# Performance work log

Hardware: AMD Instinct MI355X
Metric: run time of the kernel (lower is better)

## Reference

```python
import jax, jax.numpy as jnp
import numpy as np

N_HEAD = 8


def _axial_attn(x, wq, wk, wv, fw, fb, axis):
    # x: (B, T, H, W, C); axis is the axial axis in (B, nh, T, H, W, d): 2=T, 3=H, 4=W
    B, T, H, W, C = x.shape
    d = C // N_HEAD

    def heads(y):
        # (B,T,H,W,C) -> (B, nh, T, H, W, d)
        return jnp.moveaxis(y.reshape(B, T, H, W, N_HEAD, d), -2, 1)

    q, k, v = heads(x @ wq), heads(x @ wk), heads(x @ wv)
    # restrict attention to the axial axis: move it to -2, all other dims are batch
    q = jnp.moveaxis(q, axis, -2)
    k = jnp.moveaxis(k, axis, -2)
    v = jnp.moveaxis(v, axis, -2)
    scale = 1.0 / jnp.sqrt(jnp.asarray(d, x.dtype))
    scores = jnp.einsum('...ld,...md->...lm', q * scale, k)
    att = jax.nn.softmax(scores, axis=-1)
    o = jnp.einsum('...lm,...md->...ld', att, v)
    o = jnp.moveaxis(o, -2, axis)            # restore axial axis position
    o = jnp.moveaxis(o, 1, -2).reshape(B, T, H, W, C)  # merge heads
    return o @ fw + fb


def setup_inputs() -> dict:
    key = jax.random.key(0)
    ks = jax.random.split(key, 16)
    C = 512
    x = jax.random.normal(ks[0], (4, C, 16, 32, 32), jnp.float32)
    s = 0.02

    def w(k):
        return jax.random.normal(k, (C, C), jnp.float32) * s

    inp = {'x': x}
    i = 1
    for ax in ('w', 'h', 't'):
        inp[f'wq_{ax}'] = w(ks[i])
        inp[f'wk_{ax}'] = w(ks[i + 1])
        inp[f'wv_{ax}'] = w(ks[i + 2])
        inp[f'fc_{ax}'] = w(ks[i + 3])
        inp[f'fb_{ax}'] = jnp.zeros((C,), jnp.float32)
        i += 4
    return inp


def reference(x, wq_w, wk_w, wv_w, fc_w, fb_w,
              wq_h, wk_h, wv_h, fc_h, fb_h,
              wq_t, wk_t, wv_t, fc_t, fb_t):
    xt = jnp.moveaxis(x, 1, -1)  # (B, C, T, H, W) -> (B, T, H, W, C)
    out = (_axial_attn(xt, wq_w, wk_w, wv_w, fc_w, fb_w, 4)   # attend along W
           + _axial_attn(xt, wq_h, wk_h, wv_h, fc_h, fb_h, 3)  # attend along H
           + _axial_attn(xt, wq_t, wk_t, wv_t, fc_t, fb_t, 2))  # attend along T
    return jnp.moveaxis(out, -1, 1)  # back to (B, C, T, H, W)
```

## Files before the change

kernel.cpp:

```cpp
#include <hip/hip_runtime.h>
#include <stdint.h>

typedef __attribute__((ext_vector_type(8))) short bf16x8;
typedef __attribute__((ext_vector_type(4))) float f32x4;

static __device__ __forceinline__ short f2bf(float f) {
  uint32_t u = __builtin_bit_cast(uint32_t, f);
  u += 0x7fffu + ((u >> 16) & 1u);
  return (short)(u >> 16);
}

static __device__ __forceinline__ void gload_lds16(const void* g, void* l) {
  __builtin_amdgcn_global_load_lds((const __attribute__((address_space(1))) void*)g,
                                   (__attribute__((address_space(3))) void*)l, 16, 0, 0);
}

#define GFENCE asm volatile("" ::: "memory")

__global__ __launch_bounds__(256) void transpose_x_k(const float* __restrict__ x,
                                                     short* __restrict__ xb) {
  __shared__ float t[64][65];
  const int pt = blockIdx.x, ct = blockIdx.y, b = blockIdx.z;
  const int tid = threadIdx.x;
#pragma unroll
  for (int i = 0; i < 16; i++) {
    int cc = i * 4 + (tid >> 6);
    int pp = tid & 63;
    t[cc][pp] = x[(size_t)(b * 512 + ct * 64 + cc) * 16384 + pt * 64 + pp];
  }
  __syncthreads();
#pragma unroll
  for (int i = 0; i < 2; i++) {
    int seg = i * 256 + tid;
    int pw = seg >> 3, c8 = seg & 7;
    short tmp[8];
#pragma unroll
    for (int k = 0; k < 8; k++) tmp[k] = f2bf(t[c8 * 8 + k][pw]);
    *(uint4*)&xb[(size_t)(b * 16384 + pt * 64 + pw) * 512 + ct * 64 + c8 * 8] =
        *(const uint4*)tmp;
  }
}

struct WPtrs {
  const float* src[12];
  short* dst[12];
  int ld[12];
};

__global__ __launch_bounds__(256) void transpose_w_k(WPtrs P) {
  __shared__ float t[64][65];
  const int kt = blockIdx.x, nt = blockIdx.y, z = blockIdx.z;
  const float* src = P.src[z];
  short* dst = P.dst[z];
  const int ld = P.ld[z];
  const int tid = threadIdx.x;
#pragma unroll
  for (int i = 0; i < 16; i++) {
    int kk = i * 4 + (tid >> 6);
    int nn = tid & 63;
    t[kk][nn] = src[(kt * 64 + kk) * 512 + nt * 64 + nn];
  }
  __syncthreads();
#pragma unroll
  for (int i = 0; i < 2; i++) {
    int seg = i * 256 + tid;
    int nn = seg >> 3, k8 = seg & 7;
    short tmp[8];
#pragma unroll
    for (int k = 0; k < 8; k++) tmp[k] = f2bf(t[k8 * 8 + k][nn]);
    *(uint4*)&dst[(size_t)(nt * 64 + nn) * ld + kt * 64 + k8 * 8] = *(const uint4*)tmp;
  }
}

__global__ void bsum_k(const float* a, const float* b, const float* c, float* o) {
  int i = blockIdx.x * 256 + threadIdx.x;
  if (i < 512) o[i] = a[i] + b[i] + c[i];
}

#define LOADB(b, kh)                                                           \
  do {                                                                         \
    _Pragma("unroll") for (int ni = 0; ni < 4; ++ni) bfr[ni] =                 \
        *(const bf16x8*)(smem + ((b) * 4 + 2 + (kh)) * 16384 + boff +          \
                         ni * 1024);                                           \
  } while (0)

#define LOADA(b, kh, mq)                                                       \
  do {                                                                         \
    _Pragma("unroll") for (int mi = 0; mi < 4; ++mi) af[mi] =                  \
        *(const bf16x8*)(smem + ((b) * 4 + (kh)) * 16384 + aoff +              \
                         ((mq) * 4 + mi) * 1024);                              \
  } while (0)

#define MFMA16(mq)                                                             \
  do {                                                                         \
    __builtin_amdgcn_s_setprio(1);                                             \
    _Pragma("unroll") for (int mi = 0; mi < 4; ++mi)                           \
        _Pragma("unroll") for (int ni = 0; ni < 4; ++ni) acc[(mq) * 4 + mi]    \
            [ni] = __builtin_amdgcn_mfma_f32_16x16x32_bf16(                    \
                af[mi], bfr[ni], acc[(mq) * 4 + mi][ni], 0, 0, 0);             \
    __builtin_amdgcn_s_setprio(0);                                             \
    GFENCE;                                                                    \
  } while (0)

#define TILE(b, W0, W2, S0, S1, S2, S3)                                        \
  do {                                                                         \
    asm volatile("s_waitcnt vmcnt(" W0 ")" ::: "memory");                      \
    __builtin_amdgcn_s_barrier();                                              \
    GFENCE;                                                                    \
    LOADB(b, 0);                                                               \
    LOADA(b, 0, 0);                                                            \
    S0;                                                                        \
    MFMA16(0);                                                                 \
    __builtin_amdgcn_s_barrier();                                              \
    GFENCE;                                                                    \
    LOADA(b, 0, 1);                                                            \
    S1;                                                                        \
    MFMA16(1);                                                                 \
    asm volatile("s_waitcnt vmcnt(" W2 ")" ::: "memory");                      \
    __builtin_amdgcn_s_barrier();                                              \
    GFENCE;                                                                    \
    LOADB(b, 1);                                                               \
    LOADA(b, 1, 0);                                                            \
    S2;                                                                        \
    MFMA16(0);                                                                 \
    __builtin_amdgcn_s_barrier();                                              \
    GFENCE;                                                                    \
    LOADA(b, 1, 1);                                                            \
    S3;                                                                        \
    MFMA16(1);                                                                 \
  } while (0)

template <int MODE>
__global__ __launch_bounds__(512, 2) void gemm256_k(const short* __restrict__ A,
                                                    int lda,
                                                    const short* __restrict__ B,
                                                    int ldb, void* __restrict__ Dp,
                                                    int K, int ldd,
                                                    const float* __restrict__ bsum,
                                                    int GN) {
  extern __shared__ char smem[];
  const int tid = threadIdx.x;
  const int lane = tid & 63, wave = tid >> 6;
  const int wr = wave >> 2, wc = wave & 3;
  const int r4 = lane & 15, kl = lane >> 4;

  int bid = blockIdx.x;
  const int cpx = gridDim.x >> 3;
  bid = (bid & 7) * cpx + (bid >> 3);
  int bm, bn;
  if constexpr (MODE == 0) {
    bn = bid % GN;
    bm = bid / GN;
  } else {
    bm = bid & 1;
    bn = bid >> 1;
  }

  const int NT = K >> 6;

  const int srow = tid >> 2;
  const int schk = (tid & 3) ^ ((tid >> 4) & 3);
  const short* gA0 = A + (size_t)(bm * 256 + srow) * lda + schk * 8;
  const short* gB0 = B + (size_t)(bn * 256 + srow) * ldb + schk * 8;

  auto stage = [&](int tt, int x) {
    const short* g = (x < 2) ? gA0 : gB0;
    const size_t rstep = (size_t)128 * ((x < 2) ? lda : ldb);
    const size_t koff = (size_t)tt * 64 + (x & 1) * 32;
    char* ldst = smem + (((tt & 1) * 4 + x) * 16384) + wave * 1024;
#pragma unroll
    for (int i = 0; i < 2; ++i)
      gload_lds16(g + i * rstep + koff, ldst + i * 8192);
  };

  const int kls = kl ^ (r4 >> 2);
  const int aoff = wr * 8192 + r4 * 64 + kls * 16;
  const int boff = wc * 4096 + r4 * 64 + kls * 16;

  f32x4 acc[8][4];
#pragma unroll
  for (int i = 0; i < 8; ++i)
#pragma unroll
    for (int j = 0; j < 4; ++j) acc[i][j] = (f32x4){0.f, 0.f, 0.f, 0.f};
  bf16x8 af[4], bfr[4];

  stage(0, 0);
  stage(0, 2);
  stage(0, 1);
  stage(0, 3);
  stage(1, 0);
  stage(1, 2);

  int t = 0;
  for (; t < NT - 2; ++t) {
    const int b = t & 1;
    TILE(b, "8", "8", stage(t + 1, 1), stage(t + 1, 3), stage(t + 2, 0),
         stage(t + 2, 2));
  }
  {
    const int b = t & 1;
    TILE(b, "8", "8", stage(t + 1, 1), stage(t + 1, 3), (void)0, (void)0);
    ++t;
  }
  {
    const int b = t & 1;
    TILE(b, "4", "0", (void)0, (void)0, (void)0, (void)0);
  }

  const int m0 = wr * 128 + kl * 4;
  const int n0 = wc * 64 + r4;
  if (MODE == 0) {
    short* D = (short*)Dp;
#pragma unroll
    for (int mi = 0; mi < 8; ++mi)
#pragma unroll
      for (int ni = 0; ni < 4; ++ni)
#pragma unroll
        for (int r = 0; r < 4; ++r) {
          int row = bm * 256 + m0 + mi * 16 + r;
          int col = bn * 256 + n0 + ni * 16;
          D[(size_t)row * ldd + col] = f2bf(acc[mi][ni][r]);
        }
  } else {
    float* D = (float*)Dp + (size_t)((bn * 256) >> 14) * 8388608;
#pragma unroll
    for (int mi = 0; mi < 8; ++mi)
#pragma unroll
      for (int ni = 0; ni < 4; ++ni)
#pragma unroll
        for (int r = 0; r < 4; ++r) {
          int c = bm * 256 + m0 + mi * 16 + r;
          int n = (bn * 256 + n0 + ni * 16) & 16383;
          if (MODE == 1)
            D[(size_t)c * 16384 + n] = acc[mi][ni][r] + bsum[c];
          else
            D[(size_t)c * 16384 + n] += acc[mi][ni][r];
        }
  }
}

template <int L>
__global__ __launch_bounds__(256) void attn_k(const short* __restrict__ qkv,
                                              short* __restrict__ o, int Adiv, int Bmul,
                                              int Cmul, int stride, int obase,
                                              int ostride) {
  constexpr int R = 256 / L;
  constexpr int SPT = (L * L) / 256;
  constexpr int OPT = 64 / R;
  __shared__ short Ks[L][72];
  __shared__ short Vs[L][72];
  __shared__ short Qs[L][72];
  __shared__ float att[L][L + 1];
  const int tid = threadIdx.x;
  const int blk = blockIdx.x;
  const int s = blk >> 3, head = blk & 7;
  const int base = (s / Adiv) * Bmul + (s % Adiv) * Cmul;

  for (int idx = tid; idx < L * 8 * 3; idx += 256) {
    int part = idx / (L * 8);
    int rem = idx - part * (L * 8);
    int row = rem >> 3, seg = rem & 7;
    int n = base + row * stride;
    uint4 v = *(const uint4*)&qkv[(size_t)n * 1536 + part * 512 + head * 64 + seg * 8];
    short* dst = (part == 0 ? &Qs[row][0] : part == 1 ? &Ks[row][0] : &Vs[row][0]);
    *(uint4*)(dst + seg * 8) = v;
  }
  __syncthreads();

  const int l = tid / R, r = tid % R;
  float q[64];
#pragma unroll
  for (int w = 0; w < 8; w++) {
    uint4 u = *(const uint4*)&Qs[l][w * 8];
    uint32_t arr[4] = {u.x, u.y, u.z, u.w};
#pragma unroll
    for (int p = 0; p < 4; p++) {
      q[w * 8 + p * 2] = __builtin_bit_cast(float, arr[p] << 16);
      q[w * 8 + p * 2 + 1] = __builtin_bit_cast(float, arr[p] & 0xffff0000u);
    }
  }
  float sc[SPT];
#pragma unroll
  for (int jj = 0; jj < SPT; jj++) {
    int j = jj * R + r;
    float a0 = 0.f;
#pragma unroll
    for (int w = 0; w < 8; w++) {
      uint4 u = *(const uint4*)&Ks[j][w * 8];
      uint32_t arr[4] = {u.x, u.y, u.z, u.w};
#pragma unroll
      for (int p = 0; p < 4; p++) {
        a0 += q[w * 8 + p * 2] * __builtin_bit_cast(float, arr[p] << 16);
        a0 += q[w * 8 + p * 2 + 1] * __builtin_bit_cast(float, arr[p] & 0xffff0000u);
      }
    }
    sc[jj] = a0 * 0.125f;
  }
  float mx = sc[0];
#pragma unroll
  for (int jj = 1; jj < SPT; jj++) mx = fmaxf(mx, sc[jj]);
#pragma unroll
  for (int d = 1; d < R; d <<= 1) mx = fmaxf(mx, __shfl_xor(mx, d));
  float p_[SPT];
  float sum = 0.f;
#pragma unroll
  for (int jj = 0; jj < SPT; jj++) {
    p_[jj] = __expf(sc[jj] - mx);
    sum += p_[jj];
  }
#pragma unroll
  for (int d = 1; d < R; d <<= 1) sum += __shfl_xor(sum, d);
  float inv = 1.0f / sum;
#pragma unroll
  for (int jj = 0; jj < SPT; jj++) att[l][jj * R + r] = p_[jj] * inv;
  __syncthreads();

  float oa[OPT] = {};
#pragma unroll 4
  for (int j = 0; j < L; j++) {
    float a = att[l][j];
    if constexpr (OPT == 8) {
      uint4 u = *(const uint4*)&Vs[j][r * 8];
      uint32_t arr[4] = {u.x, u.y, u.z, u.w};
#pragma unroll
      for (int p = 0; p < 4; p++) {
        oa[p * 2] += a * __builtin_bit_cast(float, arr[p] << 16);
        oa[p * 2 + 1] += a * __builtin_bit_cast(float, arr[p] & 0xffff0000u);
      }
    } else {
      uint2 u = *(const uint2*)&Vs[j][r * 4];
      uint32_t arr[2] = {u.x, u.y};
#pragma unroll
      for (int p = 0; p < 2; p++) {
        oa[p * 2] += a * __builtin_bit_cast(float, arr[p] << 16);
        oa[p * 2 + 1] += a * __builtin_bit_cast(float, arr[p] & 0xffff0000u);
      }
    }
  }
  short tmp[OPT];
#pragma unroll
  for (int i = 0; i < OPT; i++) tmp[i] = f2bf(oa[i]);
  int n = base + l * stride;
  if constexpr (OPT == 8)
    *(uint4*)&o[(size_t)n * ostride + obase + head * 64 + r * 8] = *(const uint4*)tmp;
  else
    *(uint2*)&o[(size_t)n * ostride + obase + head * 64 + r * 4] = *(const uint2*)tmp;
}

extern "C" void kernel_launch(void* const* d_in, const int* in_sizes, int n_in,
                              void* d_out, int out_size, void* d_ws, size_t ws_size,
                              hipStream_t stream) {
  const float* x = (const float*)d_in[0];
  const float* wq[3];
  const float* wk[3];
  const float* wv[3];
  const float* fc[3];
  const float* fb[3];
  for (int a = 0; a < 3; a++) {
    wq[a] = (const float*)d_in[1 + a * 5];
    wk[a] = (const float*)d_in[2 + a * 5];
    wv[a] = (const float*)d_in[3 + a * 5];
    fc[a] = (const float*)d_in[4 + a * 5];
    fb[a] = (const float*)d_in[5 + a * 5];
  }
  char* ws = (char*)d_ws;
  short* xb = (short*)(ws);
  short* qkv = (short*)(ws + 67108864);
  short* wqkvt = (short*)(ws + 268435456);
  short* fctA = (short*)(ws + 273154048);
  float* bsum = (float*)(ws + 274726912);
  short* ob = (short*)(ws + 274728960);
  float* out = (float*)d_out;

  const bool fused = ws_size >= 476055552ull;

  (void)hipFuncSetAttribute((const void*)&gemm256_k<0>,
                            hipFuncAttributeMaxDynamicSharedMemorySize, 131072);
  (void)hipFuncSetAttribute((const void*)&gemm256_k<1>,
                            hipFuncAttributeMaxDynamicSharedMemorySize, 131072);
  (void)hipFuncSetAttribute((const void*)&gemm256_k<2>,
                            hipFuncAttributeMaxDynamicSharedMemorySize, 131072);

  WPtrs P;
  for (int a = 0; a < 3; a++) {
    P.src[a * 4 + 0] = wq[a];
    P.src[a * 4 + 1] = wk[a];
    P.src[a * 4 + 2] = wv[a];
    P.src[a * 4 + 3] = fc[a];
    P.dst[a * 4 + 0] = wqkvt + (size_t)a * 1536 * 512;
    P.dst[a * 4 + 1] = wqkvt + (size_t)a * 1536 * 512 + 512 * 512;
    P.dst[a * 4 + 2] = wqkvt + (size_t)a * 1536 * 512 + 2 * 512 * 512;
    P.dst[a * 4 + 3] = fctA + a * 512;
    P.ld[a * 4 + 0] = 512;
    P.ld[a * 4 + 1] = 512;
    P.ld[a * 4 + 2] = 512;
    P.ld[a * 4 + 3] = 1536;
  }
  transpose_w_k<<<dim3(8, 8, 12), 256, 0, stream>>>(P);
  bsum_k<<<dim3(2), 256, 0, stream>>>(fb[0], fb[1], fb[2], bsum);
  transpose_x_k<<<dim3(256, 8, 4), 256, 0, stream>>>(x, xb);

  const int Ad[3] = {1, 32, 1024};
  const int Bm_[3] = {32, 1024, 16384};
  const int Cm[3] = {0, 1, 1};
  const int St[3] = {1, 32, 1024};
  const int Ls[3] = {32, 32, 16};

  for (int a = 0; a < 3; a++) {
    gemm256_k<0><<<dim3(1536), 512, 131072, stream>>>(
        xb, 512, wqkvt + (size_t)a * 1536 * 512, 512, (void*)qkv, 512, 1536,
        nullptr, 6);
    const int obase = fused ? a * 512 : 0;
    const int ostr = fused ? 1536 : 512;
    if (Ls[a] == 32)
      attn_k<32><<<dim3(2048 * 8), 256, 0, stream>>>(qkv, ob, Ad[a], Bm_[a], Cm[a],
                                                     St[a], obase, ostr);
    else
      attn_k<16><<<dim3(4096 * 8), 256, 0, stream>>>(qkv, ob, Ad[a], Bm_[a], Cm[a],
                                                     St[a], obase, ostr);
    if (!fused) {
      if (a == 0)
        gemm256_k<1><<<dim3(512), 512, 131072, stream>>>(
            fctA + a * 512, 1536, ob, 512, (void*)out, 512, 0, bsum, 0);
      else
        gemm256_k<2><<<dim3(512), 512, 131072, stream>>>(
            fctA + a * 512, 1536, ob, 512, (void*)out, 512, 0, bsum, 0);
    }
  }
  if (fused) {
    gemm256_k<1><<<dim3(512), 512, 131072, stream>>>(
        fctA, 1536, ob, 1536, (void*)out, 1536, 0, bsum, 0);
  }
}
```

Baseline: 830.5 us.

## Restructure GEMM mainloop into 4-stage K=32 LDS pipeline with explicit waits

```diff
diff --git a/kernel.cpp b/kernel.cpp
--- a/kernel.cpp
+++ b/kernel.cpp
@@ -77,18 +77,16 @@
   if (i < 512) o[i] = a[i] + b[i] + c[i];
 }
 
-#define LOADB(b, kh)                                                           \
+#define LOADB(q)                                                               \
   do {                                                                         \
     _Pragma("unroll") for (int ni = 0; ni < 4; ++ni) bfr[ni] =                 \
-        *(const bf16x8*)(smem + ((b) * 4 + 2 + (kh)) * 16384 + boff +          \
-                         ni * 1024);                                           \
+        *(const bf16x8*)(smem + (q) * 32768 + 16384 + boff + ni * 1024);       \
   } while (0)
 
-#define LOADA(b, kh, mq)                                                       \
+#define LOADA(q, mq)                                                           \
   do {                                                                         \
     _Pragma("unroll") for (int mi = 0; mi < 4; ++mi) af[mi] =                  \
-        *(const bf16x8*)(smem + ((b) * 4 + (kh)) * 16384 + aoff +              \
-                         ((mq) * 4 + mi) * 1024);                              \
+        *(const bf16x8*)(smem + (q) * 32768 + aoff + ((mq) * 4 + mi) * 1024);  \
   } while (0)
 
 #define MFMA16(mq)                                                             \
@@ -102,33 +100,39 @@
     GFENCE;                                                                    \
   } while (0)
 
-#define TILE(b, W0, W2, S0, S1, S2, S3)                                        \
+#define PH0(q, SA)                                                             \
   do {                                                                         \
-    asm volatile("s_waitcnt vmcnt(" W0 ")" ::: "memory");                      \
+    LOADB(q);                                                                  \
+    LOADA(q, 0);                                                               \
+    SA;                                                                        \
+    GFENCE;                                                                    \
     __builtin_amdgcn_s_barrier();                                              \
-    GFENCE;                                                                    \
-    LOADB(b, 0);                                                               \
-    LOADA(b, 0, 0);                                                            \
-    S0;                                                                        \
+    asm volatile("s_waitcnt lgkmcnt(0)" ::: "memory");                         \
+    __builtin_amdgcn_sched_barrier(0);                                         \
     MFMA16(0);                                                                 \
+    GFENCE;                                                                    \
     __builtin_amdgcn_s_barrier();                                              \
     GFENCE;                                                                    \
-    LOADA(b, 0, 1);                                                            \
-    S1;                                                                        \
+  } while (0)
+
+#define PH1(q, SB, VM)                                                         \
+  do {                                                                         \
+    LOADA(q, 1);                                                               \
+    SB;                                                                        \
+    VM;                                                                        \
+    GFENCE;                                                                    \
+    __builtin_amdgcn_s_barrier();                                              \
+    asm volatile("s_waitcnt lgkmcnt(0)" ::: "memory");                         \
+    __builtin_amdgcn_sched_barrier(0);                                         \
     MFMA16(1);                                                                 \
-    asm volatile("s_waitcnt vmcnt(" W2 ")" ::: "memory");                      \
+    GFENCE;                                                                    \
     __builtin_amdgcn_s_barrier();                                              \
     GFENCE;                                                                    \
-    LOADB(b, 1);                                                               \
-    LOADA(b, 1, 0);                                                            \
-    S2;                                                                        \
-    MFMA16(0);                                                                 \
-    __builtin_amdgcn_s_barrier();                                              \
-    GFENCE;                                                                    \
-    LOADA(b, 1, 1);                                                            \
-    S3;                                                                        \
-    MFMA16(1);                                                                 \
   } while (0)
+
+#define VM8 asm volatile("s_waitcnt vmcnt(8)" ::: "memory")
+#define VM4 asm volatile("s_waitcnt vmcnt(4)" ::: "memory")
+#define VM0 asm volatile("s_waitcnt vmcnt(0)" ::: "memory")
 
 template <int MODE>
 __global__ __launch_bounds__(512, 2) void gemm256_k(const short* __restrict__ A,
@@ -156,7 +160,7 @@
     bn = bid >> 1;
   }
 
-  const int NT = K >> 6;
+  const int NT = K >> 5;
 
   const int srow = tid >> 2;
   const int schk = (tid & 3) ^ ((tid >> 4) & 3);
@@ -164,10 +168,10 @@
   const short* gB0 = B + (size_t)(bn * 256 + srow) * ldb + schk * 8;
 
   auto stage = [&](int tt, int x) {
-    const short* g = (x < 2) ? gA0 : gB0;
-    const size_t rstep = (size_t)128 * ((x < 2) ? lda : ldb);
-    const size_t koff = (size_t)tt * 64 + (x & 1) * 32;
-    char* ldst = smem + (((tt & 1) * 4 + x) * 16384) + wave * 1024;
+    const short* g = x ? gB0 : gA0;
+    const size_t rstep = (size_t)128 * (x ? ldb : lda);
+    const size_t koff = (size_t)tt * 32;
+    char* ldst = smem + (tt & 3) * 32768 + x * 16384 + wave * 1024;
 #pragma unroll
     for (int i = 0; i < 2; ++i)
       gload_lds16(g + i * rstep + koff, ldst + i * 8192);
@@ -185,26 +189,38 @@
   bf16x8 af[4], bfr[4];
 
   stage(0, 0);
-  stage(0, 2);
   stage(0, 1);
-  stage(0, 3);
   stage(1, 0);
-  stage(1, 2);
+  stage(1, 1);
+  stage(2, 0);
+  stage(2, 1);
+  VM8;
+  GFENCE;
+  __builtin_amdgcn_s_barrier();
+  GFENCE;
 
   int t = 0;
-  for (; t < NT - 2; ++t) {
-    const int b = t & 1;
-    TILE(b, "8", "8", stage(t + 1, 1), stage(t + 1, 3), stage(t + 2, 0),
-         stage(t + 2, 2));
+  for (; t < NT - 3; ++t) {
+    const int q = t & 3;
+    PH0(q, stage(t + 3, 0));
+    PH1(q, stage(t + 3, 1), VM8);
   }
   {
-    const int b = t & 1;
-    TILE(b, "8", "8", stage(t + 1, 1), stage(t + 1, 3), (void)0, (void)0);
+    const int q = t & 3;
+    PH0(q, (void)0);
+    PH1(q, (void)0, VM4);
     ++t;
   }
   {
-    const int b = t & 1;
-    TILE(b, "4", "0", (void)0, (void)0, (void)0, (void)0);
+    const int q = t & 3;
+    PH0(q, (void)0);
+    PH1(q, (void)0, VM0);
+    ++t;
+  }
+  {
+    const int q = t & 3;
+    PH0(q, (void)0);
+    PH1(q, (void)0, (void)0);
   }
 
   const int m0 = wr * 128 + kl * 4;
```

Result: no change. 843.0 us (+1.5%).

## Rewrite axial attention with per-wave MFMA tiles and always fuse output projection

Applied to the files above, without the earlier changes.

```diff
diff --git a/kernel.cpp b/kernel.cpp
--- a/kernel.cpp
+++ b/kernel.cpp
@@ -240,111 +240,124 @@
 }
 
 template <int L>
-__global__ __launch_bounds__(256) void attn_k(const short* __restrict__ qkv,
-                                              short* __restrict__ o, int Adiv, int Bmul,
-                                              int Cmul, int stride, int obase,
-                                              int ostride) {
-  constexpr int R = 256 / L;
-  constexpr int SPT = (L * L) / 256;
-  constexpr int OPT = 64 / R;
-  __shared__ short Ks[L][72];
-  __shared__ short Vs[L][72];
-  __shared__ short Qs[L][72];
-  __shared__ float att[L][L + 1];
+__global__ __launch_bounds__(256) void attn_mfma_k(const short* __restrict__ qkv,
+                                                   short* __restrict__ o, int Adiv,
+                                                   int Bmul, int Cmul, int stride,
+                                                   int obase) {
+  constexpr int MT = L / 16;
+  constexpr int PITCH = 40;
+  __shared__ short lds[4 * (32 + 64) * PITCH];
   const int tid = threadIdx.x;
-  const int blk = blockIdx.x;
-  const int s = blk >> 3, head = blk & 7;
+  const int lane = tid & 63, wave = tid >> 6;
+  short* p_lds = lds + wave * (96 * PITCH);
+  short* vt = p_lds + 32 * PITCH;
+
+  const int wid = blockIdx.x * 4 + wave;
+  const int s = wid >> 3, head = wid & 7;
   const int base = (s / Adiv) * Bmul + (s % Adiv) * Cmul;
-
-  for (int idx = tid; idx < L * 8 * 3; idx += 256) {
-    int part = idx / (L * 8);
-    int rem = idx - part * (L * 8);
-    int row = rem >> 3, seg = rem & 7;
-    int n = base + row * stride;
-    uint4 v = *(const uint4*)&qkv[(size_t)n * 1536 + part * 512 + head * 64 + seg * 8];
-    short* dst = (part == 0 ? &Qs[row][0] : part == 1 ? &Ks[row][0] : &Vs[row][0]);
-    *(uint4*)(dst + seg * 8) = v;
-  }
-  __syncthreads();
-
-  const int l = tid / R, r = tid % R;
-  float q[64];
-#pragma unroll
-  for (int w = 0; w < 8; w++) {
-    uint4 u = *(const uint4*)&Qs[l][w * 8];
-    uint32_t arr[4] = {u.x, u.y, u.z, u.w};
-#pragma unroll
-    for (int p = 0; p < 4; p++) {
-      q[w * 8 + p * 2] = __builtin_bit_cast(float, arr[p] << 16);
-      q[w * 8 + p * 2 + 1] = __builtin_bit_cast(float, arr[p] & 0xffff0000u);
+  const int r4 = lane & 15, kl = lane >> 4;
+
+  if constexpr (L == 16) {
+    for (int i = lane; i < 96 * PITCH; i += 64) p_lds[i] = 0;
+  }
+
+  bf16x8 qf[MT][2], kf[MT][2];
+#pragma unroll
+  for (int mi = 0; mi < MT; ++mi)
+#pragma unroll
+    for (int ks = 0; ks < 2; ++ks) {
+      size_t nrow = (size_t)(base + (mi * 16 + r4) * stride) * 1536 + head * 64 +
+                    ks * 32 + kl * 8;
+      qf[mi][ks] = *(const bf16x8*)&qkv[nrow];
+      kf[mi][ks] = *(const bf16x8*)&qkv[nrow + 512];
     }
-  }
-  float sc[SPT];
-#pragma unroll
-  for (int jj = 0; jj < SPT; jj++) {
-    int j = jj * R + r;
-    float a0 = 0.f;
-#pragma unroll
-    for (int w = 0; w < 8; w++) {
-      uint4 u = *(const uint4*)&Ks[j][w * 8];
-      uint32_t arr[4] = {u.x, u.y, u.z, u.w};
-#pragma unroll
-      for (int p = 0; p < 4; p++) {
-        a0 += q[w * 8 + p * 2] * __builtin_bit_cast(float, arr[p] << 16);
-        a0 += q[w * 8 + p * 2 + 1] * __builtin_bit_cast(float, arr[p] & 0xffff0000u);
-      }
+
+#pragma unroll
+  for (int it = 0; it < L / 8; ++it) {
+    int j = (lane >> 3) + it * 8;
+    uint4 u = *(const uint4*)&qkv[(size_t)(base + j * stride) * 1536 + 1024 +
+                                  head * 64 + (lane & 7) * 8];
+    ushort e[8];
+    *(uint4*)e = u;
+#pragma unroll
+    for (int q = 0; q < 8; ++q) vt[((lane & 7) * 8 + q) * PITCH + j] = (short)e[q];
+  }
+
+  f32x4 sacc[MT][MT];
+#pragma unroll
+  for (int i = 0; i < MT; ++i)
+#pragma unroll
+    for (int j = 0; j < MT; ++j) sacc[i][j] = (f32x4){0.f, 0.f, 0.f, 0.f};
+#pragma unroll
+  for (int mi = 0; mi < MT; ++mi)
+#pragma unroll
+    for (int ni = 0; ni < MT; ++ni)
+#pragma unroll
+      for (int ks = 0; ks < 2; ++ks)
+        sacc[mi][ni] = __builtin_amdgcn_mfma_f32_16x16x32_bf16(
+            qf[mi][ks], kf[ni][ks], sacc[mi][ni], 0, 0, 0);
+
+#pragma unroll
+  for (int mi = 0; mi < MT; ++mi) {
+    float mx[4], sm[4];
+#pragma unroll
+    for (int r = 0; r < 4; ++r) {
+      float m = sacc[mi][0][r];
+      if (MT == 2) m = fmaxf(m, sacc[mi][1][r]);
+#pragma unroll
+      for (int d = 1; d < 16; d <<= 1) m = fmaxf(m, __shfl_xor(m, d));
+      mx[r] = m;
     }
-    sc[jj] = a0 * 0.125f;
-  }
-  float mx = sc[0];
-#pragma unroll
-  for (int jj = 1; jj < SPT; jj++) mx = fmaxf(mx, sc[jj]);
-#pragma unroll
-  for (int d = 1; d < R; d <<= 1) mx = fmaxf(mx, __shfl_xor(mx, d));
-  float p_[SPT];
-  float sum = 0.f;
-#pragma unroll
-  for (int jj = 0; jj < SPT; jj++) {
-    p_[jj] = __expf(sc[jj] - mx);
-    sum += p_[jj];
-  }
-#pragma unroll
-  for (int d = 1; d < R; d <<= 1) sum += __shfl_xor(sum, d);
-  float inv = 1.0f / sum;
-#pragma unroll
-  for (int jj = 0; jj < SPT; jj++) att[l][jj * R + r] = p_[jj] * inv;
-  __syncthreads();
-
-  float oa[OPT] = {};
-#pragma unroll 4
-  for (int j = 0; j < L; j++) {
-    float a = att[l][j];
-    if constexpr (OPT == 8) {
-      uint4 u = *(const uint4*)&Vs[j][r * 8];
-      uint32_t arr[4] = {u.x, u.y, u.z, u.w};
-#pragma unroll
-      for (int p = 0; p < 4; p++) {
-        oa[p * 2] += a * __builtin_bit_cast(float, arr[p] << 16);
-        oa[p * 2 + 1] += a * __builtin_bit_cast(float, arr[p] & 0xffff0000u);
-      }
-    } else {
-      uint2 u = *(const uint2*)&Vs[j][r * 4];
-      uint32_t arr[2] = {u.x, u.y};
-#pragma unroll
-      for (int p = 0; p < 2; p++) {
-        oa[p * 2] += a * __builtin_bit_cast(float, arr[p] << 16);
-        oa[p * 2 + 1] += a * __builtin_bit_cast(float, arr[p] & 0xffff0000u);
-      }
+#pragma unroll
+    for (int ni = 0; ni < MT; ++ni)
+#pragma unroll
+      for (int r = 0; r < 4; ++r)
+        sacc[mi][ni][r] = __expf((sacc[mi][ni][r] - mx[r]) * 0.125f);
+#pragma unroll
+    for (int r = 0; r < 4; ++r) {
+      float t = sacc[mi][0][r];
+      if (MT == 2) t += sacc[mi][1][r];
+#pragma unroll
+      for (int d = 1; d < 16; d <<= 1) t += __shfl_xor(t, d);
+      sm[r] = 1.0f / t;
     }
-  }
-  short tmp[OPT];
-#pragma unroll
-  for (int i = 0; i < OPT; i++) tmp[i] = f2bf(oa[i]);
-  int n = base + l * stride;
-  if constexpr (OPT == 8)
-    *(uint4*)&o[(size_t)n * ostride + obase + head * 64 + r * 8] = *(const uint4*)tmp;
-  else
-    *(uint2*)&o[(size_t)n * ostride + obase + head * 64 + r * 4] = *(const uint2*)tmp;
+#pragma unroll
+    for (int ni = 0; ni < MT; ++ni)
+#pragma unroll
+      for (int r = 0; r < 4; ++r)
+        p_lds[(mi * 16 + kl * 4 + r) * PITCH + ni * 16 + r4] =
+            f2bf(sacc[mi][ni][r] * sm[r]);
+  }
+  asm volatile("s_waitcnt lgkmcnt(0)" ::: "memory");
+
+  bf16x8 paf[MT], vbf[4];
+#pragma unroll
+  for (int mi = 0; mi < MT; ++mi)
+    paf[mi] = *(const bf16x8*)&p_lds[(mi * 16 + r4) * PITCH + kl * 8];
+#pragma unroll
+  for (int nd = 0; nd < 4; ++nd)
+    vbf[nd] = *(const bf16x8*)&vt[(nd * 16 + r4) * PITCH + kl * 8];
+  f32x4 oacc[MT][4];
+#pragma unroll
+  for (int i = 0; i < MT; ++i)
+#pragma unroll
+    for (int j = 0; j < 4; ++j) oacc[i][j] = (f32x4){0.f, 0.f, 0.f, 0.f};
+#pragma unroll
+  for (int mi = 0; mi < MT; ++mi)
+#pragma unroll
+    for (int nd = 0; nd < 4; ++nd)
+      oacc[mi][nd] = __builtin_amdgcn_mfma_f32_16x16x32_bf16(paf[mi], vbf[nd],
+                                                             oacc[mi][nd], 0, 0, 0);
+
+#pragma unroll
+  for (int mi = 0; mi < MT; ++mi)
+#pragma unroll
+    for (int r = 0; r < 4; ++r) {
+      int n = base + (mi * 16 + kl * 4 + r) * stride;
+      size_t ob = (size_t)n * 1536 + obase + head * 64 + r4;
+#pragma unroll
+      for (int nd = 0; nd < 4; ++nd) o[ob + nd * 16] = f2bf(oacc[mi][nd][r]);
+    }
 }
 
 extern "C" void kernel_launch(void* const* d_in, const int* in_sizes, int n_in,
@@ -372,13 +385,9 @@
   short* ob = (short*)(ws + 274728960);
   float* out = (float*)d_out;
 
-  const bool fused = ws_size >= 476055552ull;
-
   (void)hipFuncSetAttribute((const void*)&gemm256_k<0>,
                             hipFuncAttributeMaxDynamicSharedMemorySize, 131072);
   (void)hipFuncSetAttribute((const void*)&gemm256_k<1>,
-                            hipFuncAttributeMaxDynamicSharedMemorySize, 131072);
-  (void)hipFuncSetAttribute((const void*)&gemm256_k<2>,
                             hipFuncAttributeMaxDynamicSharedMemorySize, 131072);
 
   WPtrs P;
@@ -410,25 +419,13 @@
     gemm256_k<0><<<dim3(1536), 512, 131072, stream>>>(
         xb, 512, wqkvt + (size_t)a * 1536 * 512, 512, (void*)qkv, 512, 1536,
         nullptr, 6);
-    const int obase = fused ? a * 512 : 0;
-    const int ostr = fused ? 1536 : 512;
     if (Ls[a] == 32)
-      attn_k<32><<<dim3(2048 * 8), 256, 0, stream>>>(qkv, ob, Ad[a], Bm_[a], Cm[a],
-                                                     St[a], obase, ostr);
+      attn_mfma_k<32><<<dim3(4096), 256, 0, stream>>>(qkv, ob, Ad[a], Bm_[a], Cm[a],
+                                                      St[a], a * 512);
     else
-      attn_k<16><<<dim3(4096 * 8), 256, 0, stream>>>(qkv, ob, Ad[a], Bm_[a], Cm[a],
-                                                     St[a], obase, ostr);
-    if (!fused) {
-      if (a == 0)
-        gemm256_k<1><<<dim3(512), 512, 131072, stream>>>(
-            fctA + a * 512, 1536, ob, 512, (void*)out, 512, 0, bsum, 0);
-      else
-        gemm256_k<2><<<dim3(512), 512, 131072, stream>>>(
-            fctA + a * 512, 1536, ob, 512, (void*)out, 512, 0, bsum, 0);
-    }
-  }
-  if (fused) {
-    gemm256_k<1><<<dim3(512), 512, 131072, stream>>>(
-        fctA, 1536, ob, 1536, (void*)out, 1536, 0, bsum, 0);
-  }
-}
+      attn_mfma_k<16><<<dim3(8192), 256, 0, stream>>>(qkv, ob, Ad[a], Bm_[a], Cm[a],
+                                                      St[a], a * 512);
+  }
+  gemm256_k<1><<<dim3(512), 512, 131072, stream>>>(
+      fctA, 1536, ob, 1536, (void*)out, 1536, 0, bsum, 0);
+}
```

After: 705.4 us. -15.1%, faster.
